# Performance work log

Hardware: AMD Instinct MI355X
Metric: run time of the kernel (lower is better)

## Reference

```python
import jax, jax.numpy as jnp
import numpy as np

N_NODES = 50000
N_EDGES = 800000
D_FEAT = 128
HIDDEN = 128
N_CLASSES = 16
N_GRAPHS = 64


def gcn_conv(x, src, dst, W, b, n_nodes):
    """PyG GCNConv: add self-loops, symmetric D^-1/2 (A+I) D^-1/2 normalization."""
    loop = jnp.arange(n_nodes, dtype=src.dtype)
    s = jnp.concatenate([src, loop])
    d = jnp.concatenate([dst, loop])
    deg = jax.ops.segment_sum(jnp.ones_like(d, dtype=x.dtype), d, num_segments=n_nodes)
    dinv = jnp.where(deg > 0, jax.lax.rsqrt(deg), 0.0)
    norm = dinv[s] * dinv[d]                      # [E+N]
    h = x @ W                                     # [N, H]
    msg = h[s] * norm[:, None]                    # gather + scale
    out = jax.ops.segment_sum(msg, d, num_segments=n_nodes)  # scatter-add
    return out + b


def setup_inputs() -> dict:
    key = jax.random.key(0)
    ks = jax.random.split(key, 8)
    x = jax.random.normal(ks[0], (N_NODES, D_FEAT), dtype=jnp.float32)
    edge_index = jax.random.randint(ks[1], (2, N_EDGES), 0, N_NODES, dtype=jnp.int64)
    batch = jnp.sort(jax.random.randint(ks[2], (N_NODES,), 0, N_GRAPHS, dtype=jnp.int64))
    sc = 1.0 / np.sqrt(D_FEAT)
    W1 = jax.random.normal(ks[3], (D_FEAT, HIDDEN), dtype=jnp.float32) * sc
    W2 = jax.random.normal(ks[4], (HIDDEN, HIDDEN), dtype=jnp.float32) * sc
    W3 = jax.random.normal(ks[5], (HIDDEN, HIDDEN), dtype=jnp.float32) * sc
    lin_w = jax.random.normal(ks[6], (HIDDEN, N_CLASSES), dtype=jnp.float32) * sc
    return {
        "x": x, "edge_index": edge_index, "batch": batch,
        "W1": W1, "b1": jnp.zeros((HIDDEN,), jnp.float32),
        "W2": W2, "b2": jnp.zeros((HIDDEN,), jnp.float32),
        "W3": W3, "b3": jnp.zeros((HIDDEN,), jnp.float32),
        "lin_w": lin_w, "lin_b": jnp.zeros((N_CLASSES,), jnp.float32),
    }


def reference(x, edge_index, batch, W1, b1, W2, b2, W3, b3, lin_w, lin_b):
    n = x.shape[0]
    src, dst = edge_index[0], edge_index[1]
    h = jax.nn.relu(gcn_conv(x, src, dst, W1, b1, n))
    h = jax.nn.relu(gcn_conv(h, src, dst, W2, b2, n))
    h = gcn_conv(h, src, dst, W3, b3, n)
    # global mean pool over graphs in the batch
    sums = jax.ops.segment_sum(h, batch, num_segments=N_GRAPHS)
    counts = jax.ops.segment_sum(jnp.ones((n,), h.dtype), batch, num_segments=N_GRAPHS)
    pooled = sums / jnp.maximum(counts, 1.0)[:, None]
    # dropout p=0.5 is identity at inference
    return pooled @ lin_w + lin_b
```

## Files before the change

kernel.cpp:

```cpp
#include <hip/hip_runtime.h>

#define NFEAT 128
#define NGRAPH 64
#define POOL_SPLIT 8


__device__ __forceinline__ int load_idx(const void* p, long long i, int is64) {
    return is64 ? (int)((const long long*)p)[i] : ((const int*)p)[i];
}

__global__ void detect_kernel(const unsigned int* __restrict__ ei_raw, int* __restrict__ flag) {
    __shared__ int any32;
    if (threadIdx.x == 0) any32 = 0;
    __syncthreads();
    for (int i = threadIdx.x; i < 1024; i += 256) {
        if (ei_raw[2 * i + 1] != 0u) any32 = 1;
    }
    __syncthreads();
    if (threadIdx.x == 0) *flag = any32 ? 0 : 1;
}


__global__ void deg_kernel(const void* __restrict__ ei, const int* __restrict__ flag,
                           int* __restrict__ cnt, int nE) {
    int is64 = *flag;
    int e = blockIdx.x * blockDim.x + threadIdx.x;
    if (e < nE) atomicAdd(&cnt[load_idx(ei, (long long)nE + e, is64)], 1);
}

__global__ void scanA(const int* __restrict__ cnt, int* __restrict__ row_start,
                      int* __restrict__ bsum, float* __restrict__ dinv, int n) {
    __shared__ int buf[256];
    int i = blockIdx.x * 256 + threadIdx.x;
    int v = (i < n) ? cnt[i] : 0;
    if (i < n) dinv[i] = rsqrtf((float)v + 1.0f);
    buf[threadIdx.x] = v;
    __syncthreads();
    int x = v;
    for (int off = 1; off < 256; off <<= 1) {
        int t = (threadIdx.x >= (unsigned)off) ? buf[threadIdx.x - off] : 0;
        __syncthreads();
        x += t;
        buf[threadIdx.x] = x;
        __syncthreads();
    }
    if (i < n) row_start[i] = x - v;
    if (threadIdx.x == 255) bsum[blockIdx.x] = x;
}

__global__ void scanB(int* __restrict__ bsum, int nb, int* __restrict__ total) {
    __shared__ int buf[256];
    int v = (threadIdx.x < (unsigned)nb) ? bsum[threadIdx.x] : 0;
    buf[threadIdx.x] = v;
    __syncthreads();
    int x = v;
    for (int off = 1; off < 256; off <<= 1) {
        int t = (threadIdx.x >= (unsigned)off) ? buf[threadIdx.x - off] : 0;
        __syncthreads();
        x += t;
        buf[threadIdx.x] = x;
        __syncthreads();
    }
    if (threadIdx.x < (unsigned)nb) bsum[threadIdx.x] = x - v;
    if (threadIdx.x == 255) *total = buf[255];
}

__global__ void scanC(int* __restrict__ row_start, const int* __restrict__ bsum, int n) {
    int i = blockIdx.x * 256 + threadIdx.x;
    if (i < n) row_start[i] += bsum[blockIdx.x];
}

__global__ void fill_kernel(const void* __restrict__ ei, const int* __restrict__ flag,
                            const int* __restrict__ row_start, int* __restrict__ cursor,
                            const float* __restrict__ dinv, int* __restrict__ csr_src,
                            float* __restrict__ csr_norm, int nE) {
    int is64 = *flag;
    int e = blockIdx.x * blockDim.x + threadIdx.x;
    if (e >= nE) return;
    int u = load_idx(ei, e, is64);
    int v = load_idx(ei, (long long)nE + e, is64);
    int pos = row_start[v] + atomicAdd(&cursor[v], 1);
    csr_src[pos]  = u;
    csr_norm[pos] = dinv[u] * dinv[v];
}


__global__ __launch_bounds__(256) void gemm_kernel(const float* __restrict__ in,
                                                   const float* __restrict__ W,
                                                   float* __restrict__ out, int n) {
    __shared__ float xs[8][128];
    int r0 = blockIdx.x * 8;
    for (int i = threadIdx.x; i < 8 * 128; i += 256) {
        int r = i >> 7, c = i & 127;
        xs[r][c] = (r0 + r < n) ? in[(size_t)(r0 + r) * NFEAT + c] : 0.0f;
    }
    __syncthreads();
    int c  = threadIdx.x & 127;
    int rh = threadIdx.x >> 7;
    float a0 = 0.f, a1 = 0.f, a2 = 0.f, a3 = 0.f;
#pragma unroll 4
    for (int k = 0; k < 128; k++) {
        float w = W[k * NFEAT + c];
        a0 += xs[rh * 4 + 0][k] * w;
        a1 += xs[rh * 4 + 1][k] * w;
        a2 += xs[rh * 4 + 2][k] * w;
        a3 += xs[rh * 4 + 3][k] * w;
    }
    int rb = r0 + rh * 4;
    if (rb + 0 < n) out[(size_t)(rb + 0) * NFEAT + c] = a0;
    if (rb + 1 < n) out[(size_t)(rb + 1) * NFEAT + c] = a1;
    if (rb + 2 < n) out[(size_t)(rb + 2) * NFEAT + c] = a2;
    if (rb + 3 < n) out[(size_t)(rb + 3) * NFEAT + c] = a3;
}


__global__ __launch_bounds__(256) void agg_kernel(const float* __restrict__ h,
                                                  const int* __restrict__ row_start,
                                                  const int* __restrict__ csr_src,
                                                  const float* __restrict__ csr_norm,
                                                  const float* __restrict__ dinv,
                                                  const float* __restrict__ bias,
                                                  float* __restrict__ out, int n, int do_relu) {
    int v = blockIdx.x * 4 + (threadIdx.x >> 6);
    if (v >= n) return;
    int lane = threadIdx.x & 63;
    float ax = 0.f, ay = 0.f;
    int s = row_start[v], e = row_start[v + 1];
    int i = s;
    for (; i + 3 < e; i += 4) {
        int u0 = csr_src[i + 0], u1 = csr_src[i + 1];
        int u2 = csr_src[i + 2], u3 = csr_src[i + 3];
        float n0 = csr_norm[i + 0], n1 = csr_norm[i + 1];
        float n2 = csr_norm[i + 2], n3 = csr_norm[i + 3];
        float2 h0 = *reinterpret_cast<const float2*>(h + (size_t)u0 * NFEAT + lane * 2);
        float2 h1 = *reinterpret_cast<const float2*>(h + (size_t)u1 * NFEAT + lane * 2);
        float2 h2 = *reinterpret_cast<const float2*>(h + (size_t)u2 * NFEAT + lane * 2);
        float2 h3 = *reinterpret_cast<const float2*>(h + (size_t)u3 * NFEAT + lane * 2);
        ax += n0 * h0.x + n1 * h1.x + n2 * h2.x + n3 * h3.x;
        ay += n0 * h0.y + n1 * h1.y + n2 * h2.y + n3 * h3.y;
    }
    for (; i < e; i++) {
        int u0 = csr_src[i];
        float n0 = csr_norm[i];
        float2 h0 = *reinterpret_cast<const float2*>(h + (size_t)u0 * NFEAT + lane * 2);
        ax += n0 * h0.x;
        ay += n0 * h0.y;
    }
    float dv = dinv[v];
    float nm = dv * dv;
    float2 hv = *reinterpret_cast<const float2*>(h + (size_t)v * NFEAT + lane * 2);
    ax += nm * hv.x + bias[lane * 2 + 0];
    ay += nm * hv.y + bias[lane * 2 + 1];
    if (do_relu) {
        ax = fmaxf(ax, 0.f);
        ay = fmaxf(ay, 0.f);
    }
    float2 o;
    o.x = ax;
    o.y = ay;
    *reinterpret_cast<float2*>(out + (size_t)v * NFEAT + lane * 2) = o;
}


__global__ void bounds_kernel(const void* __restrict__ batch, const int* __restrict__ flag,
                              int* __restrict__ gstart, int* __restrict__ gend, int n) {
    int is64 = *flag;
    int i = blockIdx.x * blockDim.x + threadIdx.x;
    if (i >= n) return;
    int g = load_idx(batch, i, is64);
    if (i == 0) {
        gstart[g] = 0;
    } else {
        int gp = load_idx(batch, i - 1, is64);
        if (gp != g) {
            gend[gp]  = i;
            gstart[g] = i;
        }
    }
    if (i == n - 1) gend[g] = n;
}

__global__ void pool_kernel(const float* __restrict__ B, const int* __restrict__ gstart,
                            const int* __restrict__ gend, float* __restrict__ psum) {
    int g    = blockIdx.x / POOL_SPLIT;
    int part = blockIdx.x % POOL_SPLIT;
    int c    = threadIdx.x;
    int s = gstart[g], e = gend[g];
    if (s > e) { s = 0; e = 0; }
    int len   = e - s;
    int chunk = (len + POOL_SPLIT - 1) / POOL_SPLIT;
    int ls = s + part * chunk;
    int le = min(ls + chunk, e);
    float acc = 0.f;
    for (int i = ls; i < le; i++) acc += B[(size_t)i * NFEAT + c];
    psum[((size_t)g * POOL_SPLIT + part) * NFEAT + c] = acc;
}

__global__ void pool_reduce_kernel(const float* __restrict__ psum, const int* __restrict__ gstart,
                                   const int* __restrict__ gend, float* __restrict__ pooled) {
    int g = blockIdx.x;
    int c = threadIdx.x;
    float acc = 0.f;
#pragma unroll
    for (int p = 0; p < POOL_SPLIT; p++)
        acc += psum[((size_t)g * POOL_SPLIT + p) * NFEAT + c];
    int cn = gend[g] - gstart[g];
    float denom = (cn > 0) ? (float)cn : 1.0f;
    pooled[g * NFEAT + c] = acc / denom;
}

__global__ void final_kernel(const float* __restrict__ pooled, const float* __restrict__ lw,
                             const float* __restrict__ lb, float* __restrict__ out) {
    int idx = blockIdx.x * blockDim.x + threadIdx.x;
    if (idx >= NGRAPH * 16) return;
    int g = idx >> 4, c = idx & 15;
    float acc = lb[c];
#pragma unroll 8
    for (int k = 0; k < 128; k++) acc += pooled[g * NFEAT + k] * lw[k * 16 + c];
    out[idx] = acc;
}


extern "C" void kernel_launch(void* const* d_in, const int* in_sizes, int n_in,
                              void* d_out, int out_size, void* d_ws, size_t ws_size,
                              hipStream_t stream) {
    const float* x   = (const float*)d_in[0];
    const void*  ei  = d_in[1];
    const void*  bat = d_in[2];
    const float* W1  = (const float*)d_in[3];
    const float* b1  = (const float*)d_in[4];
    const float* W2  = (const float*)d_in[5];
    const float* b2  = (const float*)d_in[6];
    const float* W3  = (const float*)d_in[7];
    const float* b3  = (const float*)d_in[8];
    const float* lw  = (const float*)d_in[9];
    const float* lb  = (const float*)d_in[10];
    float*       out = (float*)d_out;

    const int n  = in_sizes[0] / NFEAT;
    const int nE = in_sizes[1] / 2;

    char* ws = (char*)d_ws;
    size_t off = 0;
    auto alloc = [&](size_t bytes) -> char* {
        char* p = ws + off;
        off = (off + bytes + 255) & ~(size_t)255;
        return p;
    };
    int*   flag      = (int*)alloc(256);
    int*   cnt       = (int*)alloc((size_t)n * 4);
    int*   row_start = (int*)alloc((size_t)(n + 1) * 4);
    int*   cursor    = (int*)alloc((size_t)n * 4);
    int*   bsum      = (int*)alloc(1024);
    int*   csr_src   = (int*)alloc((size_t)nE * 4);
    float* csr_norm  = (float*)alloc((size_t)nE * 4);
    float* dinv      = (float*)alloc((size_t)n * 4);
    int*   gstart    = (int*)alloc(NGRAPH * 4);
    int*   gend      = (int*)alloc(NGRAPH * 4);
    float* psum      = (float*)alloc((size_t)NGRAPH * POOL_SPLIT * NFEAT * 4);
    float* pooled    = (float*)alloc(NGRAPH * NFEAT * 4);
    float* bufA      = (float*)alloc((size_t)n * NFEAT * 4);
    float* bufB      = (float*)alloc((size_t)n * NFEAT * 4);
    (void)ws_size;

    const int TB  = 256;
    const int nbE = (nE + TB - 1) / TB;
    const int nbN = (n + TB - 1) / TB;

    hipMemsetAsync(cnt, 0, (size_t)n * 4, stream);
    hipMemsetAsync(cursor, 0, (size_t)n * 4, stream);
    hipMemsetAsync(gstart, 0x7f, NGRAPH * 4, stream);
    hipMemsetAsync(gend, 0, NGRAPH * 4, stream);

    detect_kernel<<<1, 256, 0, stream>>>((const unsigned int*)ei, flag);

    deg_kernel<<<nbE, TB, 0, stream>>>(ei, flag, cnt, nE);

    scanA<<<nbN, 256, 0, stream>>>(cnt, row_start, bsum, dinv, n);
    scanB<<<1, 256, 0, stream>>>(bsum, nbN, row_start + n);
    scanC<<<nbN, 256, 0, stream>>>(row_start, bsum, n);

    fill_kernel<<<nbE, TB, 0, stream>>>(ei, flag, row_start, cursor, dinv,
                                        csr_src, csr_norm, nE);

    const int gemmBlocks = (n + 7) / 8;
    const int aggBlocks  = (n + 3) / 4;

    gemm_kernel<<<gemmBlocks, 256, 0, stream>>>(x, W1, bufA, n);
    agg_kernel<<<aggBlocks, 256, 0, stream>>>(bufA, row_start, csr_src, csr_norm,
                                              dinv, b1, bufB, n, 1);
    gemm_kernel<<<gemmBlocks, 256, 0, stream>>>(bufB, W2, bufA, n);
    agg_kernel<<<aggBlocks, 256, 0, stream>>>(bufA, row_start, csr_src, csr_norm,
                                              dinv, b2, bufB, n, 1);
    gemm_kernel<<<gemmBlocks, 256, 0, stream>>>(bufB, W3, bufA, n);
    agg_kernel<<<aggBlocks, 256, 0, stream>>>(bufA, row_start, csr_src, csr_norm,
                                              dinv, b3, bufB, n, 0);

    bounds_kernel<<<nbN, TB, 0, stream>>>(bat, flag, gstart, gend, n);
    pool_kernel<<<NGRAPH * POOL_SPLIT, NFEAT, 0, stream>>>(bufB, gstart, gend, psum);
    pool_reduce_kernel<<<NGRAPH, NFEAT, 0, stream>>>(psum, gstart, gend, pooled);

    final_kernel<<<(NGRAPH * 16 + 255) / 256, 256, 0, stream>>>(pooled, lw, lb, out);
}
```

Measured before the change: 522.2 us.

## Stage weights in shared memory with register-tiled GEMM and float4 aggregation

The GEMM now loads the full 128x128 weight matrix and a 32-row input tile into shared memory. Each thread computes a 4x4 output tile with float4 weight reads and float4 stores, which cuts global weight reloads per output row. The aggregation kernel switches from 64 lanes with float2 to 32 lanes with float4 per node, so a block handles 8 nodes and each gather instruction fetches more bytes. The cost is 80KB of shared memory per GEMM block, which limits occupancy, plus possible LDS bank conflicts on the strided xs reads.

```diff
diff --git a/kernel.cpp b/kernel.cpp
--- a/kernel.cpp
+++ b/kernel.cpp
@@ -3,6 +3,7 @@
 #define NFEAT 128
 #define NGRAPH 64
 #define POOL_SPLIT 8
+#define GR 32
 
 
 __device__ __forceinline__ int load_idx(const void* p, long long i, int is64) {
@@ -88,29 +89,46 @@
 __global__ __launch_bounds__(256) void gemm_kernel(const float* __restrict__ in,
                                                    const float* __restrict__ W,
                                                    float* __restrict__ out, int n) {
-    __shared__ float xs[8][128];
-    int r0 = blockIdx.x * 8;
-    for (int i = threadIdx.x; i < 8 * 128; i += 256) {
-        int r = i >> 7, c = i & 127;
-        xs[r][c] = (r0 + r < n) ? in[(size_t)(r0 + r) * NFEAT + c] : 0.0f;
-    }
-    __syncthreads();
-    int c  = threadIdx.x & 127;
-    int rh = threadIdx.x >> 7;
-    float a0 = 0.f, a1 = 0.f, a2 = 0.f, a3 = 0.f;
-#pragma unroll 4
+    __shared__ float Wl[128 * 128];
+    __shared__ float xs[GR][128];
+    const int t  = threadIdx.x;
+    const int r0 = blockIdx.x * GR;
+
+    for (int i = t; i < 128 * 128 / 4; i += 256)
+        ((float4*)Wl)[i] = ((const float4*)W)[i];
+    for (int i = t; i < GR * 128 / 4; i += 256) {
+        int r  = i >> 5;
+        int c4 = i & 31;
+        float4 v = make_float4(0.f, 0.f, 0.f, 0.f);
+        if (r0 + r < n) v = ((const float4*)(in + (size_t)(r0 + r) * NFEAT))[c4];
+        ((float4*)&xs[r][0])[c4] = v;
+    }
+    __syncthreads();
+
+    const int c4 = (t & 31) * 4;
+    const int r4 = (t >> 5) * 4;
+    float4 acc0 = make_float4(0.f, 0.f, 0.f, 0.f);
+    float4 acc1 = acc0, acc2 = acc0, acc3 = acc0;
+
+#pragma unroll 8
     for (int k = 0; k < 128; k++) {
-        float w = W[k * NFEAT + c];
-        a0 += xs[rh * 4 + 0][k] * w;
-        a1 += xs[rh * 4 + 1][k] * w;
-        a2 += xs[rh * 4 + 2][k] * w;
-        a3 += xs[rh * 4 + 3][k] * w;
-    }
-    int rb = r0 + rh * 4;
-    if (rb + 0 < n) out[(size_t)(rb + 0) * NFEAT + c] = a0;
-    if (rb + 1 < n) out[(size_t)(rb + 1) * NFEAT + c] = a1;
-    if (rb + 2 < n) out[(size_t)(rb + 2) * NFEAT + c] = a2;
-    if (rb + 3 < n) out[(size_t)(rb + 3) * NFEAT + c] = a3;
+        float4 wv = *(const float4*)&Wl[k * 128 + c4];
+        float x0 = xs[r4 + 0][k];
+        float x1 = xs[r4 + 1][k];
+        float x2 = xs[r4 + 2][k];
+        float x3 = xs[r4 + 3][k];
+        acc0.x += x0 * wv.x; acc0.y += x0 * wv.y; acc0.z += x0 * wv.z; acc0.w += x0 * wv.w;
+        acc1.x += x1 * wv.x; acc1.y += x1 * wv.y; acc1.z += x1 * wv.z; acc1.w += x1 * wv.w;
+        acc2.x += x2 * wv.x; acc2.y += x2 * wv.y; acc2.z += x2 * wv.z; acc2.w += x2 * wv.w;
+        acc3.x += x3 * wv.x; acc3.y += x3 * wv.y; acc3.z += x3 * wv.z; acc3.w += x3 * wv.w;
+    }
+
+    float4 a[4] = {acc0, acc1, acc2, acc3};
+#pragma unroll
+    for (int i = 0; i < 4; i++) {
+        int r = r0 + r4 + i;
+        if (r < n) *(float4*)&out[(size_t)r * NFEAT + c4] = a[i];
+    }
 }
 
 
@@ -121,10 +139,11 @@
                                                   const float* __restrict__ dinv,
                                                   const float* __restrict__ bias,
                                                   float* __restrict__ out, int n, int do_relu) {
-    int v = blockIdx.x * 4 + (threadIdx.x >> 6);
+    int v = blockIdx.x * 8 + (threadIdx.x >> 5);
     if (v >= n) return;
-    int lane = threadIdx.x & 63;
-    float ax = 0.f, ay = 0.f;
+    int lane = threadIdx.x & 31;
+    int fo   = lane * 4;
+    float4 acc = make_float4(0.f, 0.f, 0.f, 0.f);
     int s = row_start[v], e = row_start[v + 1];
     int i = s;
     for (; i + 3 < e; i += 4) {
@@ -132,33 +151,39 @@
         int u2 = csr_src[i + 2], u3 = csr_src[i + 3];
         float n0 = csr_norm[i + 0], n1 = csr_norm[i + 1];
         float n2 = csr_norm[i + 2], n3 = csr_norm[i + 3];
-        float2 h0 = *reinterpret_cast<const float2*>(h + (size_t)u0 * NFEAT + lane * 2);
-        float2 h1 = *reinterpret_cast<const float2*>(h + (size_t)u1 * NFEAT + lane * 2);
-        float2 h2 = *reinterpret_cast<const float2*>(h + (size_t)u2 * NFEAT + lane * 2);
-        float2 h3 = *reinterpret_cast<const float2*>(h + (size_t)u3 * NFEAT + lane * 2);
-        ax += n0 * h0.x + n1 * h1.x + n2 * h2.x + n3 * h3.x;
-        ay += n0 * h0.y + n1 * h1.y + n2 * h2.y + n3 * h3.y;
+        float4 h0 = *(const float4*)(h + (size_t)u0 * NFEAT + fo);
+        float4 h1 = *(const float4*)(h + (size_t)u1 * NFEAT + fo);
+        float4 h2 = *(const float4*)(h + (size_t)u2 * NFEAT + fo);
+        float4 h3 = *(const float4*)(h + (size_t)u3 * NFEAT + fo);
+        acc.x += n0 * h0.x + n1 * h1.x + n2 * h2.x + n3 * h3.x;
+        acc.y += n0 * h0.y + n1 * h1.y + n2 * h2.y + n3 * h3.y;
+        acc.z += n0 * h0.z + n1 * h1.z + n2 * h2.z + n3 * h3.z;
+        acc.w += n0 * h0.w + n1 * h1.w + n2 * h2.w + n3 * h3.w;
     }
     for (; i < e; i++) {
         int u0 = csr_src[i];
         float n0 = csr_norm[i];
-        float2 h0 = *reinterpret_cast<const float2*>(h + (size_t)u0 * NFEAT + lane * 2);
-        ax += n0 * h0.x;
-        ay += n0 * h0.y;
+        float4 h0 = *(const float4*)(h + (size_t)u0 * NFEAT + fo);
+        acc.x += n0 * h0.x;
+        acc.y += n0 * h0.y;
+        acc.z += n0 * h0.z;
+        acc.w += n0 * h0.w;
     }
     float dv = dinv[v];
     float nm = dv * dv;
-    float2 hv = *reinterpret_cast<const float2*>(h + (size_t)v * NFEAT + lane * 2);
-    ax += nm * hv.x + bias[lane * 2 + 0];
-    ay += nm * hv.y + bias[lane * 2 + 1];
+    float4 hv = *(const float4*)(h + (size_t)v * NFEAT + fo);
+    float4 bv = *(const float4*)(bias + fo);
+    acc.x += nm * hv.x + bv.x;
+    acc.y += nm * hv.y + bv.y;
+    acc.z += nm * hv.z + bv.z;
+    acc.w += nm * hv.w + bv.w;
     if (do_relu) {
-        ax = fmaxf(ax, 0.f);
-        ay = fmaxf(ay, 0.f);
-    }
-    float2 o;
-    o.x = ax;
-    o.y = ay;
-    *reinterpret_cast<float2*>(out + (size_t)v * NFEAT + lane * 2) = o;
+        acc.x = fmaxf(acc.x, 0.f);
+        acc.y = fmaxf(acc.y, 0.f);
+        acc.z = fmaxf(acc.z, 0.f);
+        acc.w = fmaxf(acc.w, 0.f);
+    }
+    *(float4*)(out + (size_t)v * NFEAT + fo) = acc;
 }
 
 
@@ -273,18 +298,15 @@
     hipMemsetAsync(gend, 0, NGRAPH * 4, stream);
 
     detect_kernel<<<1, 256, 0, stream>>>((const unsigned int*)ei, flag);
-
     deg_kernel<<<nbE, TB, 0, stream>>>(ei, flag, cnt, nE);
-
     scanA<<<nbN, 256, 0, stream>>>(cnt, row_start, bsum, dinv, n);
     scanB<<<1, 256, 0, stream>>>(bsum, nbN, row_start + n);
     scanC<<<nbN, 256, 0, stream>>>(row_start, bsum, n);
-
     fill_kernel<<<nbE, TB, 0, stream>>>(ei, flag, row_start, cursor, dinv,
                                         csr_src, csr_norm, nE);
 
-    const int gemmBlocks = (n + 7) / 8;
-    const int aggBlocks  = (n + 3) / 4;
+    const int gemmBlocks = (n + GR - 1) / GR;
+    const int aggBlocks  = (n + 7) / 8;
 
     gemm_kernel<<<gemmBlocks, 256, 0, stream>>>(x, W1, bufA, n);
     agg_kernel<<<aggBlocks, 256, 0, stream>>>(bufA, row_start, csr_src, csr_norm,
@@ -299,6 +321,5 @@
     bounds_kernel<<<nbN, TB, 0, stream>>>(bat, flag, gstart, gend, n);
     pool_kernel<<<NGRAPH * POOL_SPLIT, NFEAT, 0, stream>>>(bufB, gstart, gend, psum);
     pool_reduce_kernel<<<NGRAPH, NFEAT, 0, stream>>>(psum, gstart, gend, pooled);
-
     final_kernel<<<(NGRAPH * 16 + 255) / 256, 256, 0, stream>>>(pooled, lw, lb, out);
 }
```

After: 517.9 us. Within noise of the previous version (-0.8%).
